# Optimization experiments

Hardware: AMD Instinct MI355X
Metric: run time of the kernel (lower is better)

## Reference

```python
import jax, jax.numpy as jnp
import numpy as np

N = 50000      # nodes
E = 500000     # edges (before self-loops)
D = 384        # in_channels == hidden3*6 (residual constraint)
H1, C1 = 4, 96   # conv1: heads, out_channels  -> 384
H2, C2 = 4, 96   # conv2 -> 384
H3, C3 = 6, 64   # conv3 -> 384
B = 64           # graphs in batch
SLOPE = 0.2      # GATConv leaky_relu negative_slope (PyG default)
LN_EPS = 1e-5


def _gat_params(key, fin, heads, c, scale=0.05):
    k1, k2, k3 = jax.random.split(key, 3)
    return dict(
        W=jax.random.normal(k1, (fin, heads * c), jnp.float32) * scale,
        a_src=jax.random.normal(k2, (heads, c), jnp.float32) * scale,
        a_dst=jax.random.normal(k3, (heads, c), jnp.float32) * scale,
        b=jnp.zeros((heads * c,), jnp.float32),
    )


def setup_inputs() -> dict:
    key = jax.random.key(0)
    ks = jax.random.split(key, 8)
    x = jax.random.normal(ks[0], (N, D), jnp.float32)
    edge_index = jax.random.randint(ks[1], (2, E), 0, N).astype(jnp.int64)
    batch = jnp.sort(jax.random.randint(ks[2], (N,), 0, B)).astype(jnp.int64)
    p1 = _gat_params(ks[3], D, H1, C1)
    p2 = _gat_params(ks[4], H1 * C1, H2, C2)
    p3 = _gat_params(ks[5], H2 * C2, H3, C3)
    return {
        'x': x, 'edge_index': edge_index, 'batch': batch,
        'W1': p1['W'], 'a1_src': p1['a_src'], 'a1_dst': p1['a_dst'], 'b1': p1['b'],
        'g1': jnp.ones((H1 * C1,), jnp.float32), 'be1': jnp.zeros((H1 * C1,), jnp.float32),
        'W2': p2['W'], 'a2_src': p2['a_src'], 'a2_dst': p2['a_dst'], 'b2': p2['b'],
        'g2': jnp.ones((H2 * C2,), jnp.float32), 'be2': jnp.zeros((H2 * C2,), jnp.float32),
        'W3': p3['W'], 'a3_src': p3['a_src'], 'a3_dst': p3['a_dst'], 'b3': p3['b'],
    }


def _layer_norm(x, g, b):
    mu = jnp.mean(x, axis=-1, keepdims=True)
    var = jnp.mean(jnp.square(x - mu), axis=-1, keepdims=True)
    return (x - mu) * jax.lax.rsqrt(var + LN_EPS) * g + b


def _gat_conv(x, src, dst, W, a_src, a_dst, b, heads, c):
    # h: [N, H, C] projected features (shared W across heads, PyG-style)
    h = (x @ W).reshape(N, heads, c)
    s_src = jnp.einsum('nhc,hc->nh', h, a_src)   # [N, H]
    s_dst = jnp.einsum('nhc,hc->nh', h, a_dst)
    e = jax.nn.leaky_relu(s_src[src] + s_dst[dst], SLOPE)  # [E', H]
    # segment softmax over incoming edges of each dst (self-loops guarantee coverage)
    e_max = jax.ops.segment_max(e, dst, num_segments=N)
    e = jnp.exp(e - e_max[dst])
    denom = jax.ops.segment_sum(e, dst, num_segments=N)
    alpha = e / (denom[dst] + 1e-16)                        # [E', H]
    out = jax.ops.segment_sum(h[src] * alpha[:, :, None], dst, num_segments=N)
    return out.reshape(N, heads * c) + b


def reference(x, edge_index, batch,
              W1, a1_src, a1_dst, b1, g1, be1,
              W2, a2_src, a2_dst, b2, g2, be2,
              W3, a3_src, a3_dst, b3):
    # PyG GATConv adds self-loops by default
    ar = jnp.arange(N, dtype=edge_index.dtype)
    ei = jnp.concatenate([edge_index, jnp.stack([ar, ar])], axis=1)
    src, dst = ei[0], ei[1]

    x1 = _gat_conv(x, src, dst, W1, a1_src, a1_dst, b1, H1, C1)
    x1 = jax.nn.relu(_layer_norm(x1, g1, be1))
    x2 = _gat_conv(x1, src, dst, W2, a2_src, a2_dst, b2, H2, C2)
    x2 = jax.nn.relu(_layer_norm(x2, g2, be2))
    x3 = _gat_conv(x2, src, dst, W3, a3_src, a3_dst, b3, H3, C3)
    x3 = jax.nn.relu(x3)

    x_res = x + x3
    # global_mean_pool over batch assignment (dropout is identity at eval)
    sums = jax.ops.segment_sum(x_res, batch, num_segments=B)
    counts = jax.ops.segment_sum(jnp.ones((N,), x.dtype), batch, num_segments=B)
    return sums / jnp.maximum(counts, 1.0)[:, None]
```

## Files before the change

kernel.cpp:

```cpp
#include <hip/hip_runtime.h>

#define NNODES 50000
#define NEDGES 500000
#define DIM    384
#define NB     64
#define SLOPE  0.2f
#define LN_EPS 1e-5f
#define EPRIME (NEDGES + NNODES)
#define POOLS  16
#define SCANB  256
#define NSCB   ((NNODES + SCANB - 1) / SCANB)

typedef __attribute__((ext_vector_type(8))) short short8;
typedef __attribute__((ext_vector_type(4))) float floatx4;
typedef __attribute__((ext_vector_type(2))) float floatx2;

__device__ __forceinline__ int load_i(const void* p, long long i, int is64) {
  return is64 ? (int)((const long long*)p)[i] : ((const int*)p)[i];
}
__device__ __forceinline__ unsigned short f2bf(float f) {
  unsigned u = __float_as_uint(f);
  u += 0x7fffu + ((u >> 16) & 1u);
  return (unsigned short)(u >> 16);
}
__device__ __forceinline__ float bf2f(unsigned short u) {
  return __uint_as_float(((unsigned)u) << 16);
}

__global__ void detect_kernel(const int* __restrict__ ei32, int* __restrict__ flag) {
  __shared__ int nz;
  if (threadIdx.x == 0) nz = 0;
  __syncthreads();
  if (ei32[2 * threadIdx.x + 1] != 0) atomicAdd(&nz, 1);
  __syncthreads();
  if (threadIdx.x == 0) *flag = (nz == 0) ? 1 : 0;
}

__global__ void count_kernel(const void* __restrict__ ei, const int* __restrict__ flag,
                             int* __restrict__ deg) {
  int is64 = *flag;
  for (int i = blockIdx.x * blockDim.x + threadIdx.x; i < EPRIME; i += gridDim.x * blockDim.x) {
    int d = (i < NEDGES) ? load_i(ei, (long long)NEDGES + i, is64) : (i - NEDGES);
    atomicAdd(&deg[d], 1);
  }
}

__global__ void scan1_kernel(const int* __restrict__ deg, int* __restrict__ row_ptr,
                             int* __restrict__ btot) {
  __shared__ int buf[SCANB];
  int t = threadIdx.x, idx = blockIdx.x * SCANB + t;
  int v = (idx < NNODES) ? deg[idx] : 0;
  buf[t] = v;
  __syncthreads();
  for (int off = 1; off < SCANB; off <<= 1) {
    int x = (t >= off) ? buf[t - off] : 0;
    __syncthreads();
    buf[t] += x;
    __syncthreads();
  }
  if (idx < NNODES) row_ptr[idx] = buf[t] - v;
  if (t == SCANB - 1) btot[blockIdx.x] = buf[t];
}
__global__ void scan2_kernel(int* __restrict__ btot) {
  __shared__ int buf[256];
  int t = threadIdx.x;
  int v = (t < NSCB) ? btot[t] : 0;
  buf[t] = v;
  __syncthreads();
  for (int off = 1; off < 256; off <<= 1) {
    int x = (t >= off) ? buf[t - off] : 0;
    __syncthreads();
    buf[t] += x;
    __syncthreads();
  }
  if (t < NSCB) btot[t] = buf[t] - v;
}
__global__ void scan3_kernel(int* __restrict__ row_ptr, int* __restrict__ cursor,
                             const int* __restrict__ btot) {
  int idx = blockIdx.x * SCANB + threadIdx.x;
  if (idx < NNODES) {
    int v = row_ptr[idx] + btot[blockIdx.x];
    row_ptr[idx] = v;
    cursor[idx] = v;
  }
  if (idx == 0) row_ptr[NNODES] = EPRIME;
}

__global__ void scatter_kernel(const void* __restrict__ ei, const int* __restrict__ flag,
                               int* __restrict__ cursor, int* __restrict__ srt) {
  int is64 = *flag;
  for (int i = blockIdx.x * blockDim.x + threadIdx.x; i < EPRIME; i += gridDim.x * blockDim.x) {
    int s, d;
    if (i < NEDGES) { s = load_i(ei, i, is64); d = load_i(ei, (long long)NEDGES + i, is64); }
    else            { s = d = i - NEDGES; }
    int pos = atomicAdd(&cursor[d], 1);
    srt[pos] = s;
  }
}

__global__ void convert_x_kernel(const float* __restrict__ x, unsigned short* __restrict__ xb) {
  int i = blockIdx.x * blockDim.x + threadIdx.x;
  float4 v = ((const float4*)x)[i];
  ushort4 o;
  o.x = f2bf(v.x); o.y = f2bf(v.y); o.z = f2bf(v.z); o.w = f2bf(v.w);
  ((ushort4*)xb)[i] = o;
}

__global__ void convert_w_kernel(const float* __restrict__ W1, const float* __restrict__ W2,
                                 const float* __restrict__ W3, unsigned short* __restrict__ Wt) {
  const float* W = (blockIdx.y == 0) ? W1 : (blockIdx.y == 1) ? W2 : W3;
  unsigned short* o = Wt + (size_t)blockIdx.y * DIM * DIM;
  int n = blockIdx.x;
  int k = threadIdx.x;
  o[n * DIM + k] = f2bf(W[k * DIM + n]);
}

__global__ __launch_bounds__(256)
void gemm_bf16_kernel(const unsigned short* __restrict__ A,
                      const unsigned short* __restrict__ Bt,
                      unsigned char* __restrict__ C8, int M) {
  __shared__ unsigned short As[128 * 32];
  __shared__ unsigned short Bs[128 * 32];
  int tid = threadIdx.x;
  int lane = tid & 63;
  int wave = tid >> 6;
  int bm = blockIdx.x * 128;
  int bn = blockIdx.y * 128;
  int wm = (wave & 1) * 64;
  int wn = (wave >> 1) * 64;
  int l16 = lane & 15;
  int lq  = lane >> 4;

  floatx4 acc[4][4];
#pragma unroll
  for (int mi = 0; mi < 4; ++mi)
#pragma unroll
    for (int ni = 0; ni < 4; ++ni)
      acc[mi][ni] = (floatx4){0.f, 0.f, 0.f, 0.f};

  for (int k0 = 0; k0 < DIM; k0 += 32) {
    __syncthreads();
#pragma unroll
    for (int i = 0; i < 2; ++i) {
      int c = i * 256 + tid;
      int r = c >> 2;
      int col = (c & 3) << 3;
      int ra = bm + r; if (ra >= M) ra = M - 1;
      __builtin_amdgcn_global_load_lds(
          (const __attribute__((address_space(1))) void*)(A + (size_t)ra * DIM + k0 + col),
          (__attribute__((address_space(3))) void*)(As + c * 8), 16, 0, 0);
      __builtin_amdgcn_global_load_lds(
          (const __attribute__((address_space(1))) void*)(Bt + (size_t)(bn + r) * DIM + k0 + col),
          (__attribute__((address_space(3))) void*)(Bs + c * 8), 16, 0, 0);
    }
    __syncthreads();
    short8 av[4], bv[4];
#pragma unroll
    for (int mi = 0; mi < 4; ++mi)
      av[mi] = *(const short8*)&As[(wm + mi * 16 + l16) * 32 + lq * 8];
#pragma unroll
    for (int ni = 0; ni < 4; ++ni)
      bv[ni] = *(const short8*)&Bs[(wn + ni * 16 + l16) * 32 + lq * 8];
#pragma unroll
    for (int mi = 0; mi < 4; ++mi)
#pragma unroll
      for (int ni = 0; ni < 4; ++ni)
        acc[mi][ni] = __builtin_amdgcn_mfma_f32_16x16x32_bf16(av[mi], bv[ni], acc[mi][ni], 0, 0, 0);
  }

#pragma unroll
  for (int mi = 0; mi < 4; ++mi) {
#pragma unroll
    for (int r = 0; r < 4; ++r) {
      int row = bm + wm + mi * 16 + lq * 4 + r;
      if (row < M) {
#pragma unroll
        for (int ni = 0; ni < 4; ++ni) {
          float fv = acc[mi][ni][r];
          int pk = __builtin_amdgcn_cvt_pk_fp8_f32(fv, fv, 0, false);
          C8[(size_t)row * DIM + bn + wn + ni * 16 + l16] = (unsigned char)(pk & 0xff);
        }
      }
    }
  }
}

template <int H>
__global__ __launch_bounds__(256)
void score_kernel(const unsigned char* __restrict__ h8,
                  const float* __restrict__ asrc, const float* __restrict__ adst,
                  float* __restrict__ ssrc, float* __restrict__ sdst) {
  constexpr int LPH = 48 / H;
  int wave = threadIdx.x >> 6, lane = threadIdx.x & 63;
  int n = blockIdx.x * 4 + wave;
  bool colane = lane < 48;
  int lc = min(lane, 47);
  int j = lc * 8;

  __shared__ float r1[4][64], r2[4][64];
  float s1 = 0.f, s2 = 0.f;
  if (colane) {
    uint2 pk = *(const uint2*)(h8 + (size_t)n * DIM + j);
    floatx2 p0 = __builtin_amdgcn_cvt_pk_f32_fp8((int)pk.x, false);
    floatx2 p1 = __builtin_amdgcn_cvt_pk_f32_fp8((int)pk.x, true);
    floatx2 p2 = __builtin_amdgcn_cvt_pk_f32_fp8((int)pk.y, false);
    floatx2 p3 = __builtin_amdgcn_cvt_pk_f32_fp8((int)pk.y, true);
    float f[8] = {p0.x, p0.y, p1.x, p1.y, p2.x, p2.y, p3.x, p3.y};
    float4 a0 = *(const float4*)(asrc + j);
    float4 a1 = *(const float4*)(asrc + j + 4);
    float4 d0 = *(const float4*)(adst + j);
    float4 d1 = *(const float4*)(adst + j + 4);
    s1 = f[0]*a0.x + f[1]*a0.y + f[2]*a0.z + f[3]*a0.w
       + f[4]*a1.x + f[5]*a1.y + f[6]*a1.z + f[7]*a1.w;
    s2 = f[0]*d0.x + f[1]*d0.y + f[2]*d0.z + f[3]*d0.w
       + f[4]*d1.x + f[5]*d1.y + f[6]*d1.z + f[7]*d1.w;
  }
  r1[wave][lane] = colane ? s1 : 0.f;
  r2[wave][lane] = colane ? s2 : 0.f;
  asm volatile("s_waitcnt lgkmcnt(0)" ::: "memory");
  __builtin_amdgcn_wave_barrier();
  if (lane < H) {
    float a = 0.f;
#pragma unroll
    for (int k = 0; k < LPH; ++k) a += r1[wave][lane * LPH + k];
    ssrc[n * H + lane] = a;
  } else if (lane >= 8 && lane < 8 + H) {
    int h = lane - 8;
    float a = 0.f;
#pragma unroll
    for (int k = 0; k < LPH; ++k) a += r2[wave][h * LPH + k];
    sdst[n * H + h] = a;
  }
}

template <int H>
__global__ __launch_bounds__(256)
void wexp_kernel(const int* __restrict__ row_ptr, const int* __restrict__ srt,
                 const float* __restrict__ ssrc, const float* __restrict__ sdst,
                 float* __restrict__ walpha, float* __restrict__ dden) {
  int idx = blockIdx.x * 256 + threadIdx.x;
  if (idx >= NNODES * H) return;
  int n = idx / H, h = idx - n * H;
  int start = row_ptr[n], end = row_ptr[n + 1];
  float sd = sdst[n * H + h];
  float den = 0.f;
  for (int e = start; e < end; ++e) {
    float v = ssrc[srt[e] * H + h] + sd;
    v = fmaxf(v, SLOPE * v);
    float w = __expf(v);
    walpha[(size_t)e * H + h] = w;
    den += w;
  }
  dden[n * H + h] = den;
}

template <int H, int MODE>
__global__ __launch_bounds__(256)
void aggregate_kernel(const int* __restrict__ row_ptr, const int* __restrict__ srt,
                      const float* __restrict__ walpha, const float* __restrict__ dden,
                      const unsigned char* __restrict__ h8, const float* __restrict__ bias,
                      const float* __restrict__ gamma, const float* __restrict__ beta,
                      const unsigned short* __restrict__ xresb,
                      unsigned short* __restrict__ outb) {
  constexpr int C = DIM / H;
  int wave = threadIdx.x >> 6;
  int lane = threadIdx.x & 63;
  int n = blockIdx.x * 4 + wave;
  int start = row_ptr[n];
  int deg = row_ptr[n + 1] - start;

  bool colane = lane < 48;
  int lc = min(lane, 47);
  int j = lc * 8;
  int myhead = j / C;

  float invden = 1.f / (dden[n * H + myhead] + 1e-16f);

  float acc[8];
#pragma unroll
  for (int i = 0; i < 8; ++i) acc[i] = 0.f;

  const int* sp = srt + start;
  const float* ap = walpha + (size_t)start * H + myhead;

  auto accum = [&](uint2 pk, float w) {
    floatx2 p0 = __builtin_amdgcn_cvt_pk_f32_fp8((int)pk.x, false);
    floatx2 p1 = __builtin_amdgcn_cvt_pk_f32_fp8((int)pk.x, true);
    floatx2 p2 = __builtin_amdgcn_cvt_pk_f32_fp8((int)pk.y, false);
    floatx2 p3 = __builtin_amdgcn_cvt_pk_f32_fp8((int)pk.y, true);
    acc[0] = fmaf(w, p0.x, acc[0]); acc[1] = fmaf(w, p0.y, acc[1]);
    acc[2] = fmaf(w, p1.x, acc[2]); acc[3] = fmaf(w, p1.y, acc[3]);
    acc[4] = fmaf(w, p2.x, acc[4]); acc[5] = fmaf(w, p2.y, acc[5]);
    acc[6] = fmaf(w, p3.x, acc[6]); acc[7] = fmaf(w, p3.y, acc[7]);
  };

  int ee = 0;
  for (; ee + 4 <= deg; ee += 4) {
    int i0 = sp[ee], i1 = sp[ee + 1], i2 = sp[ee + 2], i3 = sp[ee + 3];
    int s0 = __builtin_amdgcn_readfirstlane(i0);
    int s1 = __builtin_amdgcn_readfirstlane(i1);
    int s2 = __builtin_amdgcn_readfirstlane(i2);
    int s3 = __builtin_amdgcn_readfirstlane(i3);
    uint2 k0 = *(const uint2*)(h8 + (size_t)s0 * DIM + j);
    uint2 k1 = *(const uint2*)(h8 + (size_t)s1 * DIM + j);
    uint2 k2 = *(const uint2*)(h8 + (size_t)s2 * DIM + j);
    uint2 k3 = *(const uint2*)(h8 + (size_t)s3 * DIM + j);
    float w0 = ap[(ee) * H];
    float w1 = ap[(ee + 1) * H];
    float w2 = ap[(ee + 2) * H];
    float w3 = ap[(ee + 3) * H];
    accum(k0, w0); accum(k1, w1); accum(k2, w2); accum(k3, w3);
  }
  for (; ee < deg; ++ee) {
    int su = __builtin_amdgcn_readfirstlane(sp[ee]);
    uint2 pk = *(const uint2*)(h8 + (size_t)su * DIM + j);
    accum(pk, ap[ee * H]);
  }

  float v[8];
  float4 b0 = *(const float4*)(bias + j);
  float4 b1 = *(const float4*)(bias + j + 4);
  v[0] = acc[0] * invden + b0.x; v[1] = acc[1] * invden + b0.y;
  v[2] = acc[2] * invden + b0.z; v[3] = acc[3] * invden + b0.w;
  v[4] = acc[4] * invden + b1.x; v[5] = acc[5] * invden + b1.y;
  v[6] = acc[6] * invden + b1.z; v[7] = acc[7] * invden + b1.w;

  if (MODE == 0) {
    float s1 = 0.f, s2 = 0.f;
    if (colane) {
#pragma unroll
      for (int i = 0; i < 8; ++i) { s1 += v[i]; s2 += v[i] * v[i]; }
    }
#pragma unroll
    for (int off = 32; off > 0; off >>= 1) {
      s1 += __shfl_xor(s1, off);
      s2 += __shfl_xor(s2, off);
    }
    float mu = s1 * (1.f / DIM);
    float var = s2 * (1.f / DIM) - mu * mu;
    float rs = rsqrtf(var + LN_EPS);
    if (colane) {
      float4 g0 = *(const float4*)(gamma + j);
      float4 g1 = *(const float4*)(gamma + j + 4);
      float4 e0 = *(const float4*)(beta + j);
      float4 e1 = *(const float4*)(beta + j + 4);
      float gg[8] = {g0.x, g0.y, g0.z, g0.w, g1.x, g1.y, g1.z, g1.w};
      float bb[8] = {e0.x, e0.y, e0.z, e0.w, e1.x, e1.y, e1.z, e1.w};
      ushort4 o0, o1;
      unsigned short oy[8];
#pragma unroll
      for (int i = 0; i < 8; ++i) {
        float y = (v[i] - mu) * rs * gg[i] + bb[i];
        oy[i] = f2bf(fmaxf(y, 0.f));
      }
      o0.x = oy[0]; o0.y = oy[1]; o0.z = oy[2]; o0.w = oy[3];
      o1.x = oy[4]; o1.y = oy[5]; o1.z = oy[6]; o1.w = oy[7];
      *(ushort4*)(outb + (size_t)n * DIM + j) = o0;
      *(ushort4*)(outb + (size_t)n * DIM + j + 4) = o1;
    }
  } else {
    if (colane) {
      uint4 xp = *(const uint4*)(xresb + (size_t)n * DIM + j);
      float xf[8];
      xf[0] = __uint_as_float(xp.x << 16); xf[1] = __uint_as_float(xp.x & 0xffff0000u);
      xf[2] = __uint_as_float(xp.y << 16); xf[3] = __uint_as_float(xp.y & 0xffff0000u);
      xf[4] = __uint_as_float(xp.z << 16); xf[5] = __uint_as_float(xp.z & 0xffff0000u);
      xf[6] = __uint_as_float(xp.w << 16); xf[7] = __uint_as_float(xp.w & 0xffff0000u);
      ushort4 o0, o1;
      unsigned short oy[8];
#pragma unroll
      for (int i = 0; i < 8; ++i) oy[i] = f2bf(fmaxf(v[i], 0.f) + xf[i]);
      o0.x = oy[0]; o0.y = oy[1]; o0.z = oy[2]; o0.w = oy[3];
      o1.x = oy[4]; o1.y = oy[5]; o1.z = oy[6]; o1.w = oy[7];
      *(ushort4*)(outb + (size_t)n * DIM + j) = o0;
      *(ushort4*)(outb + (size_t)n * DIM + j + 4) = o1;
    }
  }
}

__global__ void pool_kernel(const unsigned short* __restrict__ xr, const void* __restrict__ batch,
                            const int* __restrict__ flag, float* __restrict__ out) {
  int b = blockIdx.x;
  int s = blockIdx.y;
  int t = threadIdx.x;
  int is64 = *flag;
  int lo, hi;
  { int l = 0, r = NNODES;
    while (l < r) { int m = (l + r) >> 1; if (load_i(batch, m, is64) < b) l = m + 1; else r = m; }
    lo = l; }
  { int l = lo, r = NNODES;
    while (l < r) { int m = (l + r) >> 1; if (load_i(batch, m, is64) < b + 1) l = m + 1; else r = m; }
    hi = l; }
  int cnt = hi - lo;
  float inv = 1.f / (float)max(cnt, 1);
  int chunk = (cnt + POOLS - 1) / POOLS;
  int r0 = lo + s * chunk;
  int r1 = min(r0 + chunk, hi);
  float acc = 0.f;
  for (int nn = r0; nn < r1; ++nn) acc += bf2f(xr[(size_t)nn * DIM + t]);
  if (r1 > r0) atomicAdd(&out[b * DIM + t], acc * inv);
}

extern "C" void kernel_launch(void* const* d_in, const int* in_sizes, int n_in,
                              void* d_out, int out_size, void* d_ws, size_t ws_size,
                              hipStream_t stream) {
  const float* x    = (const float*)d_in[0];
  const void*  ei   = d_in[1];
  const void*  batch= d_in[2];
  const float* W1   = (const float*)d_in[3];
  const float* a1s  = (const float*)d_in[4];
  const float* a1d  = (const float*)d_in[5];
  const float* b1   = (const float*)d_in[6];
  const float* g1   = (const float*)d_in[7];
  const float* be1  = (const float*)d_in[8];
  const float* W2   = (const float*)d_in[9];
  const float* a2s  = (const float*)d_in[10];
  const float* a2d  = (const float*)d_in[11];
  const float* b2   = (const float*)d_in[12];
  const float* g2   = (const float*)d_in[13];
  const float* be2  = (const float*)d_in[14];
  const float* W3   = (const float*)d_in[15];
  const float* a3s  = (const float*)d_in[16];
  const float* a3d  = (const float*)d_in[17];
  const float* b3   = (const float*)d_in[18];
  float* out = (float*)d_out;

  char* ws = (char*)d_ws;
  size_t off = 0;
  auto alloc = [&](size_t bytes) -> void* {
    void* p = ws + off;
    off = (off + bytes + 255) & ~(size_t)255;
    return p;
  };
  int*   flag    = (int*)alloc(4);
  unsigned short* Xb = (unsigned short*)alloc((size_t)NNODES * DIM * 2);
  unsigned short* Qb = (unsigned short*)alloc((size_t)NNODES * DIM * 2);
  unsigned char*  P8 = (unsigned char*)alloc((size_t)NNODES * DIM);
  unsigned short* Wt = (unsigned short*)alloc((size_t)3 * DIM * DIM * 2);
  float* ssrc    = (float*)alloc((size_t)NNODES * 6 * 4);
  float* sdst    = (float*)alloc((size_t)NNODES * 6 * 4);
  float* walpha  = (float*)alloc((size_t)EPRIME * 6 * 4);
  float* dden    = (float*)alloc((size_t)NNODES * 6 * 4);
  int*   row_ptr = (int*)alloc((size_t)(NNODES + 1) * 4);
  int*   cursor  = (int*)alloc((size_t)NNODES * 4);
  int*   deg     = (int*)alloc((size_t)NNODES * 4);
  int*   btot    = (int*)alloc((size_t)NSCB * 4);
  int*   srt     = (int*)alloc((size_t)EPRIME * 4);

  detect_kernel<<<1, 256, 0, stream>>>((const int*)ei, flag);
  hipMemsetAsync(deg, 0, (size_t)NNODES * 4, stream);
  hipMemsetAsync(d_out, 0, (size_t)out_size * 4, stream);
  int eblocks = (EPRIME + 255) / 256;
  count_kernel<<<eblocks, 256, 0, stream>>>(ei, flag, deg);
  scan1_kernel<<<NSCB, SCANB, 0, stream>>>(deg, row_ptr, btot);
  scan2_kernel<<<1, 256, 0, stream>>>(btot);
  scan3_kernel<<<NSCB, SCANB, 0, stream>>>(row_ptr, cursor, btot);
  scatter_kernel<<<eblocks, 256, 0, stream>>>(ei, flag, cursor, srt);

  convert_x_kernel<<<(NNODES * DIM / 4 + 255) / 256, 256, 0, stream>>>(x, Xb);
  convert_w_kernel<<<dim3(DIM, 3), DIM, 0, stream>>>(W1, W2, W3, Wt);

  dim3 ggrid((NNODES + 127) / 128, DIM / 128);
  int agrid = NNODES / 4;
  int smb4 = (NNODES * 4 + 255) / 256;
  int smb6 = (NNODES * 6 + 255) / 256;

  gemm_bf16_kernel<<<ggrid, 256, 0, stream>>>(Xb, Wt, P8, NNODES);
  score_kernel<4><<<agrid, 256, 0, stream>>>(P8, a1s, a1d, ssrc, sdst);
  wexp_kernel<4><<<smb4, 256, 0, stream>>>(row_ptr, srt, ssrc, sdst, walpha, dden);
  aggregate_kernel<4, 0><<<agrid, 256, 0, stream>>>(row_ptr, srt, walpha, dden, P8, b1, g1, be1,
                                                    nullptr, Qb);
  gemm_bf16_kernel<<<ggrid, 256, 0, stream>>>(Qb, Wt + (size_t)DIM * DIM, P8, NNODES);
  score_kernel<4><<<agrid, 256, 0, stream>>>(P8, a2s, a2d, ssrc, sdst);
  wexp_kernel<4><<<smb4, 256, 0, stream>>>(row_ptr, srt, ssrc, sdst, walpha, dden);
  aggregate_kernel<4, 0><<<agrid, 256, 0, stream>>>(row_ptr, srt, walpha, dden, P8, b2, g2, be2,
                                                    nullptr, Qb);
  gemm_bf16_kernel<<<ggrid, 256, 0, stream>>>(Qb, Wt + (size_t)2 * DIM * DIM, P8, NNODES);
  score_kernel<6><<<agrid, 256, 0, stream>>>(P8, a3s, a3d, ssrc, sdst);
  wexp_kernel<6><<<smb6, 256, 0, stream>>>(row_ptr, srt, ssrc, sdst, walpha, dden);
  aggregate_kernel<6, 1><<<agrid, 256, 0, stream>>>(row_ptr, srt, walpha, dden, P8, b3, nullptr,
                                                    nullptr, Xb, Qb);
  pool_kernel<<<dim3(NB, POOLS), DIM, 0, stream>>>(Qb, batch, flag, out);
}
```

Measured before the change: 526.3 us.

## Fuse edge softmax weight computation into aggregation kernel, drop wexp pass

Removes the separate wexp kernel that wrote per-edge exp weights and per-node denominators to global memory. The aggregation kernel now gathers the source score per edge, applies leaky_relu and exp inline, and accumulates the denominator itself. It also adds an 8-edge unrolled main loop to keep more gathers in flight. This saves one launch per layer and the walpha write/read traffic, but each lane now recomputes exp redundantly across the lanes of a head and makes an extra gather into ssrc.

```diff
diff --git a/kernel.cpp b/kernel.cpp
--- a/kernel.cpp
+++ b/kernel.cpp
@@ -233,31 +233,10 @@
   }
 }
 
-template <int H>
-__global__ __launch_bounds__(256)
-void wexp_kernel(const int* __restrict__ row_ptr, const int* __restrict__ srt,
-                 const float* __restrict__ ssrc, const float* __restrict__ sdst,
-                 float* __restrict__ walpha, float* __restrict__ dden) {
-  int idx = blockIdx.x * 256 + threadIdx.x;
-  if (idx >= NNODES * H) return;
-  int n = idx / H, h = idx - n * H;
-  int start = row_ptr[n], end = row_ptr[n + 1];
-  float sd = sdst[n * H + h];
-  float den = 0.f;
-  for (int e = start; e < end; ++e) {
-    float v = ssrc[srt[e] * H + h] + sd;
-    v = fmaxf(v, SLOPE * v);
-    float w = __expf(v);
-    walpha[(size_t)e * H + h] = w;
-    den += w;
-  }
-  dden[n * H + h] = den;
-}
-
 template <int H, int MODE>
 __global__ __launch_bounds__(256)
 void aggregate_kernel(const int* __restrict__ row_ptr, const int* __restrict__ srt,
-                      const float* __restrict__ walpha, const float* __restrict__ dden,
+                      const float* __restrict__ ssrc, const float* __restrict__ sdst,
                       const unsigned char* __restrict__ h8, const float* __restrict__ bias,
                       const float* __restrict__ gamma, const float* __restrict__ beta,
                       const unsigned short* __restrict__ xresb,
@@ -274,14 +253,14 @@
   int j = lc * 8;
   int myhead = j / C;
 
-  float invden = 1.f / (dden[n * H + myhead] + 1e-16f);
+  float sd = sdst[n * H + myhead];
 
   float acc[8];
 #pragma unroll
   for (int i = 0; i < 8; ++i) acc[i] = 0.f;
+  float den = 0.f;
 
   const int* sp = srt + start;
-  const float* ap = walpha + (size_t)start * H + myhead;
 
   auto accum = [&](uint2 pk, float w) {
     floatx2 p0 = __builtin_amdgcn_cvt_pk_f32_fp8((int)pk.x, false);
@@ -293,30 +272,58 @@
     acc[4] = fmaf(w, p2.x, acc[4]); acc[5] = fmaf(w, p2.y, acc[5]);
     acc[6] = fmaf(w, p3.x, acc[6]); acc[7] = fmaf(w, p3.y, acc[7]);
   };
+  auto edge_w = [&](float f) {
+    float v = f + sd;
+    v = fmaxf(v, SLOPE * v);
+    return __expf(v);
+  };
 
   int ee = 0;
+  for (; ee + 8 <= deg; ee += 8) {
+    int s[8];
+#pragma unroll
+    for (int i = 0; i < 8; ++i) s[i] = __builtin_amdgcn_readfirstlane(sp[ee + i]);
+    uint2 k[8];
+    float f[8];
+#pragma unroll
+    for (int i = 0; i < 8; ++i) {
+      k[i] = *(const uint2*)(h8 + (size_t)s[i] * DIM + j);
+      f[i] = ssrc[s[i] * H + myhead];
+    }
+#pragma unroll
+    for (int i = 0; i < 8; ++i) {
+      float w = edge_w(f[i]);
+      den += w;
+      accum(k[i], w);
+    }
+  }
   for (; ee + 4 <= deg; ee += 4) {
-    int i0 = sp[ee], i1 = sp[ee + 1], i2 = sp[ee + 2], i3 = sp[ee + 3];
-    int s0 = __builtin_amdgcn_readfirstlane(i0);
-    int s1 = __builtin_amdgcn_readfirstlane(i1);
-    int s2 = __builtin_amdgcn_readfirstlane(i2);
-    int s3 = __builtin_amdgcn_readfirstlane(i3);
-    uint2 k0 = *(const uint2*)(h8 + (size_t)s0 * DIM + j);
-    uint2 k1 = *(const uint2*)(h8 + (size_t)s1 * DIM + j);
-    uint2 k2 = *(const uint2*)(h8 + (size_t)s2 * DIM + j);
-    uint2 k3 = *(const uint2*)(h8 + (size_t)s3 * DIM + j);
-    float w0 = ap[(ee) * H];
-    float w1 = ap[(ee + 1) * H];
-    float w2 = ap[(ee + 2) * H];
-    float w3 = ap[(ee + 3) * H];
-    accum(k0, w0); accum(k1, w1); accum(k2, w2); accum(k3, w3);
+    int s[4];
+#pragma unroll
+    for (int i = 0; i < 4; ++i) s[i] = __builtin_amdgcn_readfirstlane(sp[ee + i]);
+    uint2 k[4];
+    float f[4];
+#pragma unroll
+    for (int i = 0; i < 4; ++i) {
+      k[i] = *(const uint2*)(h8 + (size_t)s[i] * DIM + j);
+      f[i] = ssrc[s[i] * H + myhead];
+    }
+#pragma unroll
+    for (int i = 0; i < 4; ++i) {
+      float w = edge_w(f[i]);
+      den += w;
+      accum(k[i], w);
+    }
   }
   for (; ee < deg; ++ee) {
     int su = __builtin_amdgcn_readfirstlane(sp[ee]);
     uint2 pk = *(const uint2*)(h8 + (size_t)su * DIM + j);
-    accum(pk, ap[ee * H]);
-  }
-
+    float w = edge_w(ssrc[su * H + myhead]);
+    den += w;
+    accum(pk, w);
+  }
+
+  float invden = 1.f / (den + 1e-16f);
   float v[8];
   float4 b0 = *(const float4*)(bias + j);
   float4 b1 = *(const float4*)(bias + j + 4);
@@ -439,8 +446,6 @@
   unsigned short* Wt = (unsigned short*)alloc((size_t)3 * DIM * DIM * 2);
   float* ssrc    = (float*)alloc((size_t)NNODES * 6 * 4);
   float* sdst    = (float*)alloc((size_t)NNODES * 6 * 4);
-  float* walpha  = (float*)alloc((size_t)EPRIME * 6 * 4);
-  float* dden    = (float*)alloc((size_t)NNODES * 6 * 4);
   int*   row_ptr = (int*)alloc((size_t)(NNODES + 1) * 4);
   int*   cursor  = (int*)alloc((size_t)NNODES * 4);
   int*   deg     = (int*)alloc((size_t)NNODES * 4);
@@ -462,23 +467,18 @@
 
   dim3 ggrid((NNODES + 127) / 128, DIM / 128);
   int agrid = NNODES / 4;
-  int smb4 = (NNODES * 4 + 255) / 256;
-  int smb6 = (NNODES * 6 + 255) / 256;
 
   gemm_bf16_kernel<<<ggrid, 256, 0, stream>>>(Xb, Wt, P8, NNODES);
   score_kernel<4><<<agrid, 256, 0, stream>>>(P8, a1s, a1d, ssrc, sdst);
-  wexp_kernel<4><<<smb4, 256, 0, stream>>>(row_ptr, srt, ssrc, sdst, walpha, dden);
-  aggregate_kernel<4, 0><<<agrid, 256, 0, stream>>>(row_ptr, srt, walpha, dden, P8, b1, g1, be1,
+  aggregate_kernel<4, 0><<<agrid, 256, 0, stream>>>(row_ptr, srt, ssrc, sdst, P8, b1, g1, be1,
                                                     nullptr, Qb);
   gemm_bf16_kernel<<<ggrid, 256, 0, stream>>>(Qb, Wt + (size_t)DIM * DIM, P8, NNODES);
   score_kernel<4><<<agrid, 256, 0, stream>>>(P8, a2s, a2d, ssrc, sdst);
-  wexp_kernel<4><<<smb4, 256, 0, stream>>>(row_ptr, srt, ssrc, sdst, walpha, dden);
-  aggregate_kernel<4, 0><<<agrid, 256, 0, stream>>>(row_ptr, srt, walpha, dden, P8, b2, g2, be2,
+  aggregate_kernel<4, 0><<<agrid, 256, 0, stream>>>(row_ptr, srt, ssrc, sdst, P8, b2, g2, be2,
                                                     nullptr, Qb);
   gemm_bf16_kernel<<<ggrid, 256, 0, stream>>>(Qb, Wt + (size_t)2 * DIM * DIM, P8, NNODES);
   score_kernel<6><<<agrid, 256, 0, stream>>>(P8, a3s, a3d, ssrc, sdst);
-  wexp_kernel<6><<<smb6, 256, 0, stream>>>(row_ptr, srt, ssrc, sdst, walpha, dden);
-  aggregate_kernel<6, 1><<<agrid, 256, 0, stream>>>(row_ptr, srt, walpha, dden, P8, b3, nullptr,
+  aggregate_kernel<6, 1><<<agrid, 256, 0, stream>>>(row_ptr, srt, ssrc, sdst, P8, b3, nullptr,
                                                     nullptr, Xb, Qb);
   pool_kernel<<<dim3(NB, POOLS), DIM, 0, stream>>>(Qb, batch, flag, out);
 }
```

Result: no change. 528.3 us (+0.4%).

## Make attention weight exp edge-parallel and compute softmax denominator in aggregate

Applied to the files above, without the earlier changes.

Replaces the per-(node,head) serial loop that computed exp weights and the softmax denominator with an edge-parallel kernel. It reads source and destination scores via a new per-edge destination array written during scatter. The denominator is now accumulated inside the aggregate kernel from the weights it already loads, which removes the dden buffer. This is meant to fix load imbalance and the serial strided loop, at the cost of an extra edge-sized int array write and read.

```diff
diff --git a/kernel.cpp b/kernel.cpp
--- a/kernel.cpp
+++ b/kernel.cpp
@@ -87,7 +87,8 @@
 }
 
 __global__ void scatter_kernel(const void* __restrict__ ei, const int* __restrict__ flag,
-                               int* __restrict__ cursor, int* __restrict__ srt) {
+                               int* __restrict__ cursor, int* __restrict__ srt,
+                               int* __restrict__ dstE) {
   int is64 = *flag;
   for (int i = blockIdx.x * blockDim.x + threadIdx.x; i < EPRIME; i += gridDim.x * blockDim.x) {
     int s, d;
@@ -95,6 +96,7 @@
     else            { s = d = i - NEDGES; }
     int pos = atomicAdd(&cursor[d], 1);
     srt[pos] = s;
+    dstE[pos] = d;
   }
 }
 
@@ -235,29 +237,45 @@
 
 template <int H>
 __global__ __launch_bounds__(256)
-void wexp_kernel(const int* __restrict__ row_ptr, const int* __restrict__ srt,
-                 const float* __restrict__ ssrc, const float* __restrict__ sdst,
-                 float* __restrict__ walpha, float* __restrict__ dden) {
-  int idx = blockIdx.x * 256 + threadIdx.x;
-  if (idx >= NNODES * H) return;
-  int n = idx / H, h = idx - n * H;
-  int start = row_ptr[n], end = row_ptr[n + 1];
-  float sd = sdst[n * H + h];
-  float den = 0.f;
-  for (int e = start; e < end; ++e) {
-    float v = ssrc[srt[e] * H + h] + sd;
+void wexp_edge_kernel(const int* __restrict__ srt, const int* __restrict__ dstE,
+                      const float* __restrict__ ssrc, const float* __restrict__ sdst,
+                      float* __restrict__ walpha) {
+  int i = blockIdx.x * 256 + threadIdx.x;
+  if (i >= EPRIME) return;
+  int s = srt[i];
+  int d = dstE[i];
+  auto wfun = [](float v) {
     v = fmaxf(v, SLOPE * v);
-    float w = __expf(v);
-    walpha[(size_t)e * H + h] = w;
-    den += w;
-  }
-  dden[n * H + h] = den;
+    return __expf(v);
+  };
+  if (H == 4) {
+    float4 a = *(const float4*)(ssrc + (size_t)s * 4);
+    float4 b = *(const float4*)(sdst + (size_t)d * 4);
+    float4 o;
+    o.x = wfun(a.x + b.x);
+    o.y = wfun(a.y + b.y);
+    o.z = wfun(a.z + b.z);
+    o.w = wfun(a.w + b.w);
+    *(float4*)(walpha + (size_t)i * 4) = o;
+  } else {
+    const floatx2* pa = (const floatx2*)(ssrc + (size_t)s * 6);
+    const floatx2* pb = (const floatx2*)(sdst + (size_t)d * 6);
+    floatx2* po = (floatx2*)(walpha + (size_t)i * 6);
+#pragma unroll
+    for (int k = 0; k < 3; ++k) {
+      floatx2 a = pa[k], b = pb[k];
+      floatx2 o;
+      o.x = wfun(a.x + b.x);
+      o.y = wfun(a.y + b.y);
+      po[k] = o;
+    }
+  }
 }
 
 template <int H, int MODE>
 __global__ __launch_bounds__(256)
 void aggregate_kernel(const int* __restrict__ row_ptr, const int* __restrict__ srt,
-                      const float* __restrict__ walpha, const float* __restrict__ dden,
+                      const float* __restrict__ walpha,
                       const unsigned char* __restrict__ h8, const float* __restrict__ bias,
                       const float* __restrict__ gamma, const float* __restrict__ beta,
                       const unsigned short* __restrict__ xresb,
@@ -274,11 +292,10 @@
   int j = lc * 8;
   int myhead = j / C;
 
-  float invden = 1.f / (dden[n * H + myhead] + 1e-16f);
-
   float acc[8];
 #pragma unroll
   for (int i = 0; i < 8; ++i) acc[i] = 0.f;
+  float den = 0.f;
 
   const int* sp = srt + start;
   const float* ap = walpha + (size_t)start * H + myhead;
@@ -309,14 +326,18 @@
     float w1 = ap[(ee + 1) * H];
     float w2 = ap[(ee + 2) * H];
     float w3 = ap[(ee + 3) * H];
+    den += w0; den += w1; den += w2; den += w3;
     accum(k0, w0); accum(k1, w1); accum(k2, w2); accum(k3, w3);
   }
   for (; ee < deg; ++ee) {
     int su = __builtin_amdgcn_readfirstlane(sp[ee]);
     uint2 pk = *(const uint2*)(h8 + (size_t)su * DIM + j);
-    accum(pk, ap[ee * H]);
-  }
-
+    float w = ap[ee * H];
+    den += w;
+    accum(pk, w);
+  }
+
+  float invden = 1.f / (den + 1e-16f);
   float v[8];
   float4 b0 = *(const float4*)(bias + j);
   float4 b1 = *(const float4*)(bias + j + 4);
@@ -440,12 +461,12 @@
   float* ssrc    = (float*)alloc((size_t)NNODES * 6 * 4);
   float* sdst    = (float*)alloc((size_t)NNODES * 6 * 4);
   float* walpha  = (float*)alloc((size_t)EPRIME * 6 * 4);
-  float* dden    = (float*)alloc((size_t)NNODES * 6 * 4);
   int*   row_ptr = (int*)alloc((size_t)(NNODES + 1) * 4);
   int*   cursor  = (int*)alloc((size_t)NNODES * 4);
   int*   deg     = (int*)alloc((size_t)NNODES * 4);
   int*   btot    = (int*)alloc((size_t)NSCB * 4);
   int*   srt     = (int*)alloc((size_t)EPRIME * 4);
+  int*   dstE    = (int*)alloc((size_t)EPRIME * 4);
 
   detect_kernel<<<1, 256, 0, stream>>>((const int*)ei, flag);
   hipMemsetAsync(deg, 0, (size_t)NNODES * 4, stream);
@@ -455,30 +476,28 @@
   scan1_kernel<<<NSCB, SCANB, 0, stream>>>(deg, row_ptr, btot);
   scan2_kernel<<<1, 256, 0, stream>>>(btot);
   scan3_kernel<<<NSCB, SCANB, 0, stream>>>(row_ptr, cursor, btot);
-  scatter_kernel<<<eblocks, 256, 0, stream>>>(ei, flag, cursor, srt);
+  scatter_kernel<<<eblocks, 256, 0, stream>>>(ei, flag, cursor, srt, dstE);
 
   convert_x_kernel<<<(NNODES * DIM / 4 + 255) / 256, 256, 0, stream>>>(x, Xb);
   convert_w_kernel<<<dim3(DIM, 3), DIM, 0, stream>>>(W1, W2, W3, Wt);
 
   dim3 ggrid((NNODES + 127) / 128, DIM / 128);
   int agrid = NNODES / 4;
-  int smb4 = (NNODES * 4 + 255) / 256;
-  int smb6 = (NNODES * 6 + 255) / 256;
 
   gemm_bf16_kernel<<<ggrid, 256, 0, stream>>>(Xb, Wt, P8, NNODES);
   score_kernel<4><<<agrid, 256, 0, stream>>>(P8, a1s, a1d, ssrc, sdst);
-  wexp_kernel<4><<<smb4, 256, 0, stream>>>(row_ptr, srt, ssrc, sdst, walpha, dden);
-  aggregate_kernel<4, 0><<<agrid, 256, 0, stream>>>(row_ptr, srt, walpha, dden, P8, b1, g1, be1,
+  wexp_edge_kernel<4><<<eblocks, 256, 0, stream>>>(srt, dstE, ssrc, sdst, walpha);
+  aggregate_kernel<4, 0><<<agrid, 256, 0, stream>>>(row_ptr, srt, walpha, P8, b1, g1, be1,
                                                     nullptr, Qb);
   gemm_bf16_kernel<<<ggrid, 256, 0, stream>>>(Qb, Wt + (size_t)DIM * DIM, P8, NNODES);
   score_kernel<4><<<agrid, 256, 0, stream>>>(P8, a2s, a2d, ssrc, sdst);
-  wexp_kernel<4><<<smb4, 256, 0, stream>>>(row_ptr, srt, ssrc, sdst, walpha, dden);
-  aggregate_kernel<4, 0><<<agrid, 256, 0, stream>>>(row_ptr, srt, walpha, dden, P8, b2, g2, be2,
+  wexp_edge_kernel<4><<<eblocks, 256, 0, stream>>>(srt, dstE, ssrc, sdst, walpha);
+  aggregate_kernel<4, 0><<<agrid, 256, 0, stream>>>(row_ptr, srt, walpha, P8, b2, g2, be2,
                                                     nullptr, Qb);
   gemm_bf16_kernel<<<ggrid, 256, 0, stream>>>(Qb, Wt + (size_t)2 * DIM * DIM, P8, NNODES);
   score_kernel<6><<<agrid, 256, 0, stream>>>(P8, a3s, a3d, ssrc, sdst);
-  wexp_kernel<6><<<smb6, 256, 0, stream>>>(row_ptr, srt, ssrc, sdst, walpha, dden);
-  aggregate_kernel<6, 1><<<agrid, 256, 0, stream>>>(row_ptr, srt, walpha, dden, P8, b3, nullptr,
+  wexp_edge_kernel<6><<<eblocks, 256, 0, stream>>>(srt, dstE, ssrc, sdst, walpha);
+  aggregate_kernel<6, 1><<<agrid, 256, 0, stream>>>(row_ptr, srt, walpha, P8, b3, nullptr,
                                                     nullptr, Xb, Qb);
   pool_kernel<<<dim3(NB, POOLS), DIM, 0, stream>>>(Qb, batch, flag, out);
 }
```

Result: faster. 511.6 us (-2.8%).
